# Optimization experiments

Measured on AMD Instinct MI355X. Metric: run time of the kernel, lower is better.

## Reference

```python
import jax, jax.numpy as jnp
import numpy as np

D_MODEL = 1024
NUM_HEADS = 16
HEAD_DIM = D_MODEL // NUM_HEADS
BATCH = 2
SEQ = 2048


def setup_inputs() -> dict:
    key = jax.random.key(0)
    ks = jax.random.split(key, 9)
    s_in = 1.0 / np.sqrt(D_MODEL)  # kaiming-ish fan-in scaling for stability
    return {
        "x": jax.random.normal(ks[0], (BATCH, SEQ, D_MODEL), jnp.float32),
        "wq": jax.random.normal(ks[1], (D_MODEL, D_MODEL), jnp.float32) * s_in,
        "bq": jnp.zeros((D_MODEL,), jnp.float32),
        "wk": jax.random.normal(ks[2], (D_MODEL, D_MODEL), jnp.float32) * s_in,
        "bk": jnp.zeros((D_MODEL,), jnp.float32),
        "wv": jax.random.normal(ks[3], (D_MODEL, D_MODEL), jnp.float32) * s_in,
        "bv": jnp.zeros((D_MODEL,), jnp.float32),
        "wo": jax.random.normal(ks[4], (D_MODEL, D_MODEL), jnp.float32) * s_in,
        "bo": jnp.zeros((D_MODEL,), jnp.float32),
    }


def reference(x, wq, bq, wk, bk, wv, bv, wo, bo):
    B, S, _ = x.shape
    # QKV projections, split heads: [B, H, S, Dh]
    def proj(w, b):
        y = x @ w + b
        return y.reshape(B, S, NUM_HEADS, HEAD_DIM).transpose(0, 2, 1, 3)

    q = proj(wq, bq)
    k = proj(wk, bk)
    v = proj(wv, bv)

    scale = 1.0 / jnp.sqrt(jnp.float32(HEAD_DIM))
    scores = jnp.einsum("bhsd,bhtd->bhst", q, k) * scale  # [B,H,S,S]
    attn = jax.nn.softmax(scores, axis=-1)
    out = jnp.einsum("bhst,bhtd->bhsd", attn, v)  # [B,H,S,Dh]
    out = out.transpose(0, 2, 1, 3).reshape(B, S, D_MODEL)
    return out @ wo + bo
```

## Files before the change

### kernel.cpp

```cpp
#include <hip/hip_runtime.h>
#include <stdint.h>
#include <stddef.h>


typedef __attribute__((ext_vector_type(8))) short short8;
typedef __attribute__((ext_vector_type(4))) float f32x4;
typedef __attribute__((ext_vector_type(16))) float f32x16;
typedef __attribute__((ext_vector_type(4))) unsigned short u16x4;
typedef _Float16 h4 __attribute__((ext_vector_type(4)));

#define MFMA16(a, b, c) __builtin_amdgcn_mfma_f32_16x16x32_bf16((a), (b), (c), 0, 0, 0)
#define MFMA32(a, b, c) __builtin_amdgcn_mfma_f32_32x32x16_bf16((a), (b), (c), 0, 0, 0)
#define AS1 __attribute__((address_space(1)))
#define AS3 __attribute__((address_space(3)))

__device__ __forceinline__ unsigned short f2bf(float f) {
  union { float f; unsigned u; } v; v.f = f;
  unsigned r = v.u + 0x7fffu + ((v.u >> 16) & 1u);
  return (unsigned short)(r >> 16);
}

__device__ __forceinline__ float fexp2(float x) {
#if __has_builtin(__builtin_amdgcn_exp2f)
  return __builtin_amdgcn_exp2f(x);
#else
  return __builtin_exp2f(x);
#endif
}

__device__ __forceinline__ unsigned cvt_pk_bf16(float lo, float hi) {
  unsigned r;
  asm("v_cvt_pk_bf16_f32 %0, %1, %2" : "=v"(r) : "v"(lo), "v"(hi));
  return r;
}

__device__ __forceinline__ void pl32_swap(unsigned& a, unsigned& b) {
  asm volatile("v_permlane32_swap_b32 %0, %1" : "+v"(a), "+v"(b));
}

__device__ __forceinline__ short8 mk8(unsigned a, unsigned b, unsigned c, unsigned d) {
  union { unsigned u[4]; short8 s; } v;
  v.u[0] = a; v.u[1] = b; v.u[2] = c; v.u[3] = d;
  return v.s;
}

__global__ __launch_bounds__(256) void prep_all_kernel(const float* __restrict__ x,
                                                       const float* __restrict__ wq,
                                                       const float* __restrict__ wk,
                                                       const float* __restrict__ wv,
                                                       const float* __restrict__ wo,
                                                       const float* __restrict__ bq,
                                                       const float* __restrict__ bk,
                                                       const float* __restrict__ bv,
                                                       unsigned short* __restrict__ xb,
                                                       unsigned short* __restrict__ wt,
                                                       float* __restrict__ bias3) {
  __shared__ unsigned short t_lds[32][33];
  const int bid = blockIdx.x;
  if (bid < 4096) {
    int wsel = bid >> 10;
    int rem = bid & 1023;
    int kb = (rem >> 5) << 5;
    int nb = (rem & 31) << 5;
    const float* W = (wsel == 0) ? wq : (wsel == 1) ? wk : (wsel == 2) ? wv : wo;
    int t = threadIdx.x;
    int r = t >> 3, c = (t & 7) * 4;
    float4 v = *reinterpret_cast<const float4*>(W + (size_t)(kb + r) * 1024 + nb + c);
    t_lds[r][c + 0] = f2bf(v.x);
    t_lds[r][c + 1] = f2bf(v.y);
    t_lds[r][c + 2] = f2bf(v.z);
    t_lds[r][c + 3] = f2bf(v.w);
    __syncthreads();
    u16x4 o;
    o.x = t_lds[c + 0][r]; o.y = t_lds[c + 1][r];
    o.z = t_lds[c + 2][r]; o.w = t_lds[c + 3][r];
    *reinterpret_cast<u16x4*>(wt + (size_t)(wsel * 1024 + nb + r) * 1024 + kb + c) = o;
  } else if (bid < 8192) {
    int i = ((bid - 4096) * 256 + threadIdx.x) * 4;
    float4 v = *reinterpret_cast<const float4*>(x + i);
    u16x4 o;
    o.x = f2bf(v.x); o.y = f2bf(v.y); o.z = f2bf(v.z); o.w = f2bf(v.w);
    *reinterpret_cast<u16x4*>(xb + i) = o;
  } else {
#pragma unroll
    for (int k = 0; k < 12; ++k) {
      int i = k * 256 + threadIdx.x;
      bias3[i] = (i < 1024) ? bq[i] : (i < 2048) ? bk[i - 1024] : bv[i - 2048];
    }
  }
}

template <typename OutT, bool QS>
__global__ __launch_bounds__(256) void gemm_bt_kernel(const unsigned short* __restrict__ A,
                                                      const unsigned short* __restrict__ Bt,
                                                      const float* __restrict__ bias,
                                                      OutT* __restrict__ C, int N) {
  constexpr int K = 1024;
  __shared__ __align__(16) unsigned short a_lds[2][128 * 32];
  __shared__ __align__(16) unsigned short b_lds[2][128 * 32];
  const int nb = N >> 7;
  const int nwg = nb << 5;
  const int cpx = nwg >> 3;
  const int wg = ((int)blockIdx.x & 7) * cpx + ((int)blockIdx.x >> 3);
  const int bm = wg / nb;
  const int bn = wg % nb;
  const int m0 = bm << 7, n0 = bn << 7;
  const int tid = threadIdx.x;
  const int w = tid >> 6, l = tid & 63;
  const int lr = l & 15, lg = l >> 4;
  const int wm = (w >> 1) << 6, wn = (w & 1) << 6;

  const int q0 = w * 2, q1 = w * 2 + 1;
  const unsigned short* pa0 = A + (size_t)(m0 + q0 * 16 + (l >> 2)) * K + (l & 3) * 8;
  const unsigned short* pa1 = A + (size_t)(m0 + q1 * 16 + (l >> 2)) * K + (l & 3) * 8;
  const unsigned short* pb0 = Bt + (size_t)(n0 + q0 * 16 + (l >> 2)) * K + (l & 3) * 8;
  const unsigned short* pb1 = Bt + (size_t)(n0 + q1 * 16 + (l >> 2)) * K + (l & 3) * 8;

#define GEMM_STAGE(buf, k0)                                                        \
  do {                                                                             \
    __builtin_amdgcn_global_load_lds((const AS1 void*)(pa0 + (k0)),                \
        (AS3 void*)(&a_lds[buf][q0 * 512]), 16, 0, 0);                             \
    __builtin_amdgcn_global_load_lds((const AS1 void*)(pa1 + (k0)),                \
        (AS3 void*)(&a_lds[buf][q1 * 512]), 16, 0, 0);                             \
    __builtin_amdgcn_global_load_lds((const AS1 void*)(pb0 + (k0)),                \
        (AS3 void*)(&b_lds[buf][q0 * 512]), 16, 0, 0);                             \
    __builtin_amdgcn_global_load_lds((const AS1 void*)(pb1 + (k0)),                \
        (AS3 void*)(&b_lds[buf][q1 * 512]), 16, 0, 0);                             \
  } while (0)

  f32x4 acc[4][4] = {};
  GEMM_STAGE(0, 0);
  __syncthreads();

  int cur = 0;
  for (int k0 = 0; k0 < K; k0 += 32) {
    if (k0 + 32 < K) GEMM_STAGE(cur ^ 1, k0 + 32);
    short8 af[4], bfr[4];
#pragma unroll
    for (int i = 0; i < 4; ++i)
      af[i] = *reinterpret_cast<const short8*>(&a_lds[cur][(wm + i * 16 + lr) * 32 + lg * 8]);
#pragma unroll
    for (int i = 0; i < 4; ++i)
      bfr[i] = *reinterpret_cast<const short8*>(&b_lds[cur][(wn + i * 16 + lr) * 32 + lg * 8]);
#pragma unroll
    for (int i = 0; i < 4; ++i)
#pragma unroll
      for (int j = 0; j < 4; ++j)
        acc[i][j] = MFMA16(af[i], bfr[j], acc[i][j]);
    __syncthreads();
    cur ^= 1;
  }
#undef GEMM_STAGE

  const float scale = (QS && n0 < 1024) ? 0.18033688011111f : 1.0f;
#pragma unroll
  for (int i = 0; i < 4; ++i) {
#pragma unroll
    for (int j = 0; j < 4; ++j) {
#pragma unroll
      for (int r = 0; r < 4; ++r) {
        int m = m0 + wm + i * 16 + lg * 4 + r;
        int n = n0 + wn + j * 16 + lr;
        float val = (acc[i][j][r] + bias[n]) * scale;
        if constexpr (sizeof(OutT) == 2) {
          C[(size_t)m * N + n] = (OutT)f2bf(val);
        } else {
          C[(size_t)m * N + n] = val;
        }
      }
    }
  }
}

__device__ __forceinline__ void stage_v(char* vw, int pi, int vd0, short8 va, short8 vb) {
  union { short8 s; unsigned u[4]; } ua, ub;
  ua.s = va; ub.s = vb;
#pragma unroll
  for (int jr = 0; jr < 4; ++jr) {
    unsigned w0 = __builtin_amdgcn_perm(ub.u[jr], ua.u[jr], 0x05040100u);
    unsigned w1 = __builtin_amdgcn_perm(ub.u[jr], ua.u[jr], 0x07060302u);
    int d0 = vd0 + 2 * jr, d1 = d0 + 1;
    *reinterpret_cast<unsigned*>(vw + d0 * 128 + ((4 * pi) ^ ((d0 & 7) << 4))) = w0;
    *reinterpret_cast<unsigned*>(vw + d1 * 128 + ((4 * pi) ^ ((d1 & 7) << 4))) = w1;
  }
}

template <int S>
__global__ __launch_bounds__(256, 4) void attn_kernel(const unsigned short* __restrict__ qkv,
                                                      _Float16* __restrict__ poA,
                                                      _Float16* __restrict__ poB,
                                                      float* __restrict__ pl) {
  constexpr int TLEN = 2048 / S;
  __shared__ __align__(16) unsigned short k_lds[2][64 * 64];
  __shared__ __align__(16) unsigned short vt_lds[2][64 * 64];
  const int tid = threadIdx.x;
  const int w = tid >> 6, l = tid & 63;
  const int lq = l & 31;
  const int hi = l >> 5;
  const int nwg = 512 * S;
  const int wg = ((int)blockIdx.x & 7) * (nwg >> 3) + ((int)blockIdx.x >> 3);
  int bh, qblk, kv;
  if (S == 2) { bh = wg >> 5; qblk = (wg >> 1) & 15; kv = wg & 1; }
  else        { bh = wg >> 4; qblk = wg & 15;        kv = 0; }
  const int b = bh >> 4, h = bh & 15;
  const size_t rowbase = (size_t)b * 2048;
  const int q0 = qblk * 128 + w * 32;

  short8 qf[4];
  {
    const unsigned short* qrow = qkv + (rowbase + q0 + lq) * 3072 + h * 64 + hi * 8;
#pragma unroll
    for (int c = 0; c < 4; ++c)
      qf[c] = *reinterpret_cast<const short8*>(qrow + c * 16);
  }

  const int colsw = (16 * (l & 7)) ^ ((l >> 3) << 4);
  const char* ksrc = (const char*)(qkv + (rowbase + kv * TLEN) * 3072 + 1024 + h * 64) +
                     (size_t)(16 * w + (l >> 3)) * 6144 + colsw;
  const int kdst = w * 2048;

  const int pi = tid & 31;
  const int vd0 = (tid >> 5) * 8;
  const unsigned short* vbase = qkv + (rowbase + kv * TLEN) * 3072 + 2048 + h * 64;
  const int swz_lq = (lq & 7) << 4;

  short8 ones;
  {
    union { unsigned u[4]; short8 s; } o_;
    o_.u[0] = o_.u[1] = o_.u[2] = o_.u[3] = 0x3F803F80u;
    ones = o_.s;
  }

  f32x16 ot0 = {}, ot1 = {}, lacc = {};

  __builtin_amdgcn_global_load_lds((const AS1 void*)ksrc,
                                   (AS3 void*)((char*)k_lds[0] + kdst), 16, 0, 0);
  __builtin_amdgcn_global_load_lds((const AS1 void*)(ksrc + 49152),
                                   (AS3 void*)((char*)k_lds[0] + kdst + 1024), 16, 0, 0);
  ksrc += 393216;
  {
    short8 va = *reinterpret_cast<const short8*>(vbase + (size_t)(2 * pi) * 3072 + vd0);
    short8 vb = *reinterpret_cast<const short8*>(vbase + (size_t)(2 * pi + 1) * 3072 + vd0);
    stage_v((char*)vt_lds[0], pi, vd0, va, vb);
  }

  int cur = 0;
  for (int t0 = 0; t0 < TLEN; t0 += 64) {
    __syncthreads();
    const bool more = (t0 + 64) < TLEN;
    short8 vna, vnb;
    if (more) {
      char* kd = (char*)k_lds[cur ^ 1] + kdst;
      __builtin_amdgcn_global_load_lds((const AS1 void*)ksrc, (AS3 void*)kd, 16, 0, 0);
      __builtin_amdgcn_global_load_lds((const AS1 void*)(ksrc + 49152),
                                       (AS3 void*)(kd + 1024), 16, 0, 0);
      ksrc += 393216;
      vna = *reinterpret_cast<const short8*>(vbase + (size_t)(t0 + 64 + 2 * pi) * 3072 + vd0);
      vnb = *reinterpret_cast<const short8*>(vbase + (size_t)(t0 + 65 + 2 * pi) * 3072 + vd0);
    }
    const char* kl = (const char*)k_lds[cur];
    const char* vl = (const char*)vt_lds[cur];

    f32x16 s0 = {}, s1 = {};
    __builtin_amdgcn_s_setprio(1);
#pragma unroll
    for (int c = 0; c < 4; ++c) {
      short8 kf0 = *reinterpret_cast<const short8*>(kl + lq * 128 + ((c * 32 + hi * 16) ^ swz_lq));
      short8 kf1 = *reinterpret_cast<const short8*>(kl + (32 + lq) * 128 + ((c * 32 + hi * 16) ^ swz_lq));
      s0 = MFMA32(kf0, qf[c], s0);
      s1 = MFMA32(kf1, qf[c], s1);
    }
    __builtin_amdgcn_s_setprio(0);

    if (more) stage_v((char*)vt_lds[cur ^ 1], pi, vd0, vna, vnb);

#pragma unroll
    for (int c = 0; c < 4; ++c) {
      float t0_, t1_, t2_, t3_, t4_, t5_, t6_, t7_;
      if (c < 2) {
        const int o = c * 8;
        t0_ = fexp2(s0[o + 0]); t1_ = fexp2(s0[o + 1]);
        t2_ = fexp2(s0[o + 2]); t3_ = fexp2(s0[o + 3]);
        t4_ = fexp2(s0[o + 4]); t5_ = fexp2(s0[o + 5]);
        t6_ = fexp2(s0[o + 6]); t7_ = fexp2(s0[o + 7]);
      } else {
        const int o = (c - 2) * 8;
        t0_ = fexp2(s1[o + 0]); t1_ = fexp2(s1[o + 1]);
        t2_ = fexp2(s1[o + 2]); t3_ = fexp2(s1[o + 3]);
        t4_ = fexp2(s1[o + 4]); t5_ = fexp2(s1[o + 5]);
        t6_ = fexp2(s1[o + 6]); t7_ = fexp2(s1[o + 7]);
      }
      unsigned a0 = cvt_pk_bf16(t0_, t1_), a1 = cvt_pk_bf16(t4_, t5_);
      unsigned b0 = cvt_pk_bf16(t2_, t3_), b1 = cvt_pk_bf16(t6_, t7_);
      pl32_swap(a0, a1); pl32_swap(b0, b1);
      short8 pfc = mk8(a0, b0, a1, b1);
      short8 vf0 = *reinterpret_cast<const short8*>(vl + lq * 128 + ((c * 32 + hi * 16) ^ swz_lq));
      short8 vf1 = *reinterpret_cast<const short8*>(vl + (32 + lq) * 128 + ((c * 32 + hi * 16) ^ swz_lq));
      __builtin_amdgcn_s_setprio(1);
      ot0 = MFMA32(vf0, pfc, ot0);
      ot1 = MFMA32(vf1, pfc, ot1);
      lacc = MFMA32(ones, pfc, lacc);
      __builtin_amdgcn_s_setprio(0);
    }
    cur ^= 1;
  }

  const int g = bh * 16 + qblk;
  _Float16* pop = (kv == 0 ? poA : poB) + (size_t)g * 8192;
#pragma unroll
  for (int r = 0; r < 16; ++r) {
    int d = (r & 3) + 8 * (r >> 2) + 4 * hi;
    pop[d * 128 + w * 32 + lq] = (_Float16)ot0[r];
    pop[(32 + d) * 128 + w * 32 + lq] = (_Float16)ot1[r];
  }
  if (hi == 0) pl[(size_t)(g * S + kv) * 128 + w * 32 + lq] = lacc[0];
}

template <int S>
__global__ __launch_bounds__(256) void merge_kernel(const _Float16* __restrict__ poA,
                                                    const _Float16* __restrict__ poB,
                                                    const float* __restrict__ pl,
                                                    unsigned short* __restrict__ aout) {
  __shared__ unsigned short lo[128][72];
  const int g = blockIdx.x;
  const int bh = g >> 4, qblk = g & 15;
  const int b = bh >> 4, h = bh & 15;
  const int tid = threadIdx.x;
  const int qi = (tid & 31) * 4;
  const int dg = tid >> 5;
  const _Float16* P0 = poA + (size_t)g * 8192;
  const _Float16* P1 = poB + (size_t)g * 8192;
  const float* L = pl + (size_t)g * S * 128;

  float inv[4];
#pragma unroll
  for (int j = 0; j < 4; ++j) {
    float lv = L[qi + j];
    if (S == 2) lv += L[128 + qi + j];
    inv[j] = 1.0f / lv;
  }
#pragma unroll
  for (int dd = 0; dd < 8; ++dd) {
    int d = dg * 8 + dd;
    h4 a = *reinterpret_cast<const h4*>(P0 + d * 128 + qi);
    float o[4];
#pragma unroll
    for (int j = 0; j < 4; ++j) o[j] = (float)a[j];
    if (S == 2) {
      h4 bb = *reinterpret_cast<const h4*>(P1 + d * 128 + qi);
#pragma unroll
      for (int j = 0; j < 4; ++j) o[j] += (float)bb[j];
    }
#pragma unroll
    for (int j = 0; j < 4; ++j) lo[qi + j][d] = f2bf(o[j] * inv[j]);
  }
  __syncthreads();
  const int q = tid >> 1, c0 = (tid & 1) * 32;
  unsigned short* orow = aout + (size_t)(b * 2048 + qblk * 128 + q) * 1024 + h * 64 + c0;
#pragma unroll
  for (int k = 0; k < 4; ++k)
    *reinterpret_cast<short8*>(orow + k * 8) =
        *reinterpret_cast<const short8*>(&lo[q][c0 + k * 8]);
}

extern "C" void kernel_launch(void* const* d_in, const int* in_sizes, int n_in,
                              void* d_out, int out_size, void* d_ws, size_t ws_size,
                              hipStream_t stream) {
  const float* x  = (const float*)d_in[0];
  const float* wq = (const float*)d_in[1];
  const float* bq = (const float*)d_in[2];
  const float* wk = (const float*)d_in[3];
  const float* bk = (const float*)d_in[4];
  const float* wv = (const float*)d_in[5];
  const float* bv = (const float*)d_in[6];
  const float* wo = (const float*)d_in[7];
  const float* bo = (const float*)d_in[8];
  float* out = (float*)d_out;

  char* ws = (char*)d_ws;
  unsigned short* xb    = (unsigned short*)(ws);
  _Float16*       poA   = (_Float16*)(ws);
  unsigned short* wt    = (unsigned short*)(ws + 8388608);
  float*          bias3 = (float*)(ws + 16777216);
  unsigned short* qkvb  = (unsigned short*)(ws + 16842752);
  unsigned short* aob   = qkvb;
  _Float16*       poB   = (_Float16*)(ws + 42008576);
  const bool s2 = ws_size >= (size_t)51500000;
  float* pl = (float*)(s2 ? (ws + 50397184) : (ws + 42008576));

  prep_all_kernel<<<8193, 256, 0, stream>>>(x, wq, wk, wv, wo, bq, bk, bv, xb, wt, bias3);

  gemm_bt_kernel<unsigned short, true><<<768, 256, 0, stream>>>(xb, wt, bias3, qkvb, 3072);

  if (s2) {
    attn_kernel<2><<<1024, 256, 0, stream>>>(qkvb, poA, poB, pl);
    merge_kernel<2><<<512, 256, 0, stream>>>(poA, poB, pl, aob);
  } else {
    attn_kernel<1><<<512, 256, 0, stream>>>(qkvb, poA, poB, pl);
    merge_kernel<1><<<512, 256, 0, stream>>>(poA, poB, pl, aob);
  }

  gemm_bt_kernel<float, false><<<256, 256, 0, stream>>>(aob, wt + (size_t)3072 * 1024, bo, out, 1024);
}
```

Baseline: 125.0 us.

## Split KV inside workgroup and merge partial attention outputs in LDS

Attention now runs as one 512-thread workgroup per query block. Two groups of four waves each process half of the key/value sequence. The partial outputs and row sums are combined through LDS at the end, and the normalized bf16 result is written straight to the attention output buffer. This removes the separate merge kernel, its launch, and the fp16 partial-output round trip through global memory. In exchange it uses 64KB of LDS per workgroup with larger blocks, which may limit occupancy, and adds extra barriers for the in-LDS reduction.

Measured after the change: 116.0 us. -7.2%, faster.

```diff
diff --git a/kernel.cpp b/kernel.cpp
--- a/kernel.cpp
+++ b/kernel.cpp
@@ -7,7 +7,6 @@
 typedef __attribute__((ext_vector_type(4))) float f32x4;
 typedef __attribute__((ext_vector_type(16))) float f32x16;
 typedef __attribute__((ext_vector_type(4))) unsigned short u16x4;
-typedef _Float16 h4 __attribute__((ext_vector_type(4)));
 
 #define MFMA16(a, b, c) __builtin_amdgcn_mfma_f32_16x16x32_bf16((a), (b), (c), 0, 0, 0)
 #define MFMA32(a, b, c) __builtin_amdgcn_mfma_f32_32x32x16_bf16((a), (b), (c), 0, 0, 0)
@@ -185,26 +184,20 @@
   }
 }
 
-template <int S>
-__global__ __launch_bounds__(256, 4) void attn_kernel(const unsigned short* __restrict__ qkv,
-                                                      _Float16* __restrict__ poA,
-                                                      _Float16* __restrict__ poB,
-                                                      float* __restrict__ pl) {
-  constexpr int TLEN = 2048 / S;
-  __shared__ __align__(16) unsigned short k_lds[2][64 * 64];
-  __shared__ __align__(16) unsigned short vt_lds[2][64 * 64];
+__global__ __launch_bounds__(512, 4) void attn_kernel(const unsigned short* __restrict__ qkv,
+                                                       unsigned short* __restrict__ aout) {
+  __shared__ __align__(16) char lds[65536];
   const int tid = threadIdx.x;
   const int w = tid >> 6, l = tid & 63;
+  const int kv = w >> 2, wsub = w & 3;
   const int lq = l & 31;
   const int hi = l >> 5;
-  const int nwg = 512 * S;
-  const int wg = ((int)blockIdx.x & 7) * (nwg >> 3) + ((int)blockIdx.x >> 3);
-  int bh, qblk, kv;
-  if (S == 2) { bh = wg >> 5; qblk = (wg >> 1) & 15; kv = wg & 1; }
-  else        { bh = wg >> 4; qblk = wg & 15;        kv = 0; }
+  const int wg = ((int)blockIdx.x & 7) * 64 + ((int)blockIdx.x >> 3);
+  const int bh = wg >> 4, qblk = wg & 15;
   const int b = bh >> 4, h = bh & 15;
   const size_t rowbase = (size_t)b * 2048;
-  const int q0 = qblk * 128 + w * 32;
+  const int q0 = qblk * 128 + wsub * 32;
+  const int base = kv << 15;
 
   short8 qf[4];
   {
@@ -215,13 +208,13 @@
   }
 
   const int colsw = (16 * (l & 7)) ^ ((l >> 3) << 4);
-  const char* ksrc = (const char*)(qkv + (rowbase + kv * TLEN) * 3072 + 1024 + h * 64) +
-                     (size_t)(16 * w + (l >> 3)) * 6144 + colsw;
-  const int kdst = w * 2048;
+  const char* ksrc = (const char*)(qkv + (rowbase + kv * 1024) * 3072 + 1024 + h * 64) +
+                     (size_t)(16 * wsub + (l >> 3)) * 6144 + colsw;
+  const int kdst = wsub * 2048;
 
   const int pi = tid & 31;
-  const int vd0 = (tid >> 5) * 8;
-  const unsigned short* vbase = qkv + (rowbase + kv * TLEN) * 3072 + 2048 + h * 64;
+  const int vd0 = ((tid >> 5) & 7) * 8;
+  const unsigned short* vbase = qkv + (rowbase + kv * 1024) * 3072 + 2048 + h * 64;
   const int swz_lq = (lq & 7) << 4;
 
   short8 ones;
@@ -234,23 +227,23 @@
   f32x16 ot0 = {}, ot1 = {}, lacc = {};
 
   __builtin_amdgcn_global_load_lds((const AS1 void*)ksrc,
-                                   (AS3 void*)((char*)k_lds[0] + kdst), 16, 0, 0);
+                                   (AS3 void*)(lds + base + kdst), 16, 0, 0);
   __builtin_amdgcn_global_load_lds((const AS1 void*)(ksrc + 49152),
-                                   (AS3 void*)((char*)k_lds[0] + kdst + 1024), 16, 0, 0);
+                                   (AS3 void*)(lds + base + kdst + 1024), 16, 0, 0);
   ksrc += 393216;
   {
     short8 va = *reinterpret_cast<const short8*>(vbase + (size_t)(2 * pi) * 3072 + vd0);
     short8 vb = *reinterpret_cast<const short8*>(vbase + (size_t)(2 * pi + 1) * 3072 + vd0);
-    stage_v((char*)vt_lds[0], pi, vd0, va, vb);
+    stage_v(lds + base + 16384, pi, vd0, va, vb);
   }
 
   int cur = 0;
-  for (int t0 = 0; t0 < TLEN; t0 += 64) {
+  for (int t0 = 0; t0 < 1024; t0 += 64) {
     __syncthreads();
-    const bool more = (t0 + 64) < TLEN;
+    const bool more = (t0 + 64) < 1024;
     short8 vna, vnb;
     if (more) {
-      char* kd = (char*)k_lds[cur ^ 1] + kdst;
+      char* kd = lds + base + ((cur ^ 1) << 13) + kdst;
       __builtin_amdgcn_global_load_lds((const AS1 void*)ksrc, (AS3 void*)kd, 16, 0, 0);
       __builtin_amdgcn_global_load_lds((const AS1 void*)(ksrc + 49152),
                                        (AS3 void*)(kd + 1024), 16, 0, 0);
@@ -258,8 +251,8 @@
       vna = *reinterpret_cast<const short8*>(vbase + (size_t)(t0 + 64 + 2 * pi) * 3072 + vd0);
       vnb = *reinterpret_cast<const short8*>(vbase + (size_t)(t0 + 65 + 2 * pi) * 3072 + vd0);
     }
-    const char* kl = (const char*)k_lds[cur];
-    const char* vl = (const char*)vt_lds[cur];
+    const char* kl = lds + base + (cur << 13);
+    const char* vl = lds + base + 16384 + (cur << 13);
 
     f32x16 s0 = {}, s1 = {};
     __builtin_amdgcn_s_setprio(1);
@@ -272,7 +265,7 @@
     }
     __builtin_amdgcn_s_setprio(0);
 
-    if (more) stage_v((char*)vt_lds[cur ^ 1], pi, vd0, vna, vnb);
+    if (more) stage_v(lds + base + 16384 + ((cur ^ 1) << 13), pi, vd0, vna, vnb);
 
 #pragma unroll
     for (int c = 0; c < 4; ++c) {
@@ -305,62 +298,48 @@
     cur ^= 1;
   }
 
-  const int g = bh * 16 + qblk;
-  _Float16* pop = (kv == 0 ? poA : poB) + (size_t)g * 8192;
-#pragma unroll
-  for (int r = 0; r < 16; ++r) {
-    int d = (r & 3) + 8 * (r >> 2) + 4 * hi;
-    pop[d * 128 + w * 32 + lq] = (_Float16)ot0[r];
-    pop[(32 + d) * 128 + w * 32 + lq] = (_Float16)ot1[r];
-  }
-  if (hi == 0) pl[(size_t)(g * S + kv) * 128 + w * 32 + lq] = lacc[0];
-}
-
-template <int S>
-__global__ __launch_bounds__(256) void merge_kernel(const _Float16* __restrict__ poA,
-                                                    const _Float16* __restrict__ poB,
-                                                    const float* __restrict__ pl,
-                                                    unsigned short* __restrict__ aout) {
-  __shared__ unsigned short lo[128][72];
-  const int g = blockIdx.x;
-  const int bh = g >> 4, qblk = g & 15;
-  const int b = bh >> 4, h = bh & 15;
-  const int tid = threadIdx.x;
-  const int qi = (tid & 31) * 4;
-  const int dg = tid >> 5;
-  const _Float16* P0 = poA + (size_t)g * 8192;
-  const _Float16* P1 = poB + (size_t)g * 8192;
-  const float* L = pl + (size_t)g * S * 128;
-
-  float inv[4];
-#pragma unroll
-  for (int j = 0; j < 4; ++j) {
-    float lv = L[qi + j];
-    if (S == 2) lv += L[128 + qi + j];
-    inv[j] = 1.0f / lv;
-  }
-#pragma unroll
-  for (int dd = 0; dd < 8; ++dd) {
-    int d = dg * 8 + dd;
-    h4 a = *reinterpret_cast<const h4*>(P0 + d * 128 + qi);
-    float o[4];
-#pragma unroll
-    for (int j = 0; j < 4; ++j) o[j] = (float)a[j];
-    if (S == 2) {
-      h4 bb = *reinterpret_cast<const h4*>(P1 + d * 128 + qi);
-#pragma unroll
-      for (int j = 0; j < 4; ++j) o[j] += (float)bb[j];
-    }
-#pragma unroll
-    for (int j = 0; j < 4; ++j) lo[qi + j][d] = f2bf(o[j] * inv[j]);
-  }
   __syncthreads();
-  const int q = tid >> 1, c0 = (tid & 1) * 32;
-  unsigned short* orow = aout + (size_t)(b * 2048 + qblk * 128 + q) * 1024 + h * 64 + c0;
-#pragma unroll
-  for (int k = 0; k < 4; ++k)
-    *reinterpret_cast<short8*>(orow + k * 8) =
-        *reinterpret_cast<const short8*>(&lo[q][c0 + k * 8]);
+  float* lbuf = (float*)lds;
+  if (kv == 1) {
+    float* ob = (float*)(lds + 32768 + wsub * 8192);
+#pragma unroll
+    for (int r = 0; r < 16; ++r) {
+      int d = (r & 3) + 8 * (r >> 2) + 4 * hi;
+      ob[d * 32 + lq] = ot0[r];
+      ob[(32 + d) * 32 + lq] = ot1[r];
+    }
+    if (hi == 0) lbuf[wsub * 32 + lq] = lacc[0];
+  }
+  __syncthreads();
+  if (kv == 0) {
+    const float* ob = (const float*)(lds + 32768 + wsub * 8192);
+    const float inv = 1.0f / (lacc[0] + lbuf[wsub * 32 + lq]);
+    char* st = lds + 8192;
+    const int qq = wsub * 32 + lq;
+    const int swz = (qq & 7) << 4;
+#pragma unroll
+    for (int r = 0; r < 16; r += 2) {
+      int d = (r & 3) + 8 * (r >> 2) + 4 * hi;
+      float a0 = (ot0[r] + ob[d * 32 + lq]) * inv;
+      float a1 = (ot0[r + 1] + ob[(d + 1) * 32 + lq]) * inv;
+      *(unsigned*)(st + qq * 128 + ((2 * d) ^ swz)) = cvt_pk_bf16(a0, a1);
+      float b0_ = (ot1[r] + ob[(32 + d) * 32 + lq]) * inv;
+      float b1_ = (ot1[r + 1] + ob[(33 + d) * 32 + lq]) * inv;
+      *(unsigned*)(st + qq * 128 + ((2 * (32 + d)) ^ swz)) = cvt_pk_bf16(b0_, b1_);
+    }
+  }
+  __syncthreads();
+  {
+    int row = tid >> 2;
+    int c2 = (tid & 3) * 2;
+    int swzr = (row & 7) << 4;
+    const char* src = lds + 8192 + row * 128;
+    short8 v0 = *reinterpret_cast<const short8*>(src + ((c2 * 16) ^ swzr));
+    short8 v1 = *reinterpret_cast<const short8*>(src + (((c2 + 1) * 16) ^ swzr));
+    unsigned short* orow = aout + (rowbase + qblk * 128 + row) * 1024 + h * 64 + c2 * 8;
+    *reinterpret_cast<short8*>(orow) = v0;
+    *reinterpret_cast<short8*>(orow + 8) = v1;
+  }
 }
 
 extern "C" void kernel_launch(void* const* d_in, const int* in_sizes, int n_in,
@@ -379,26 +358,16 @@
 
   char* ws = (char*)d_ws;
   unsigned short* xb    = (unsigned short*)(ws);
-  _Float16*       poA   = (_Float16*)(ws);
+  unsigned short* aob   = (unsigned short*)(ws);
   unsigned short* wt    = (unsigned short*)(ws + 8388608);
   float*          bias3 = (float*)(ws + 16777216);
   unsigned short* qkvb  = (unsigned short*)(ws + 16842752);
-  unsigned short* aob   = qkvb;
-  _Float16*       poB   = (_Float16*)(ws + 42008576);
-  const bool s2 = ws_size >= (size_t)51500000;
-  float* pl = (float*)(s2 ? (ws + 50397184) : (ws + 42008576));
 
   prep_all_kernel<<<8193, 256, 0, stream>>>(x, wq, wk, wv, wo, bq, bk, bv, xb, wt, bias3);
 
   gemm_bt_kernel<unsigned short, true><<<768, 256, 0, stream>>>(xb, wt, bias3, qkvb, 3072);
 
-  if (s2) {
-    attn_kernel<2><<<1024, 256, 0, stream>>>(qkvb, poA, poB, pl);
-    merge_kernel<2><<<512, 256, 0, stream>>>(poA, poB, pl, aob);
-  } else {
-    attn_kernel<1><<<512, 256, 0, stream>>>(qkvb, poA, poB, pl);
-    merge_kernel<1><<<512, 256, 0, stream>>>(poA, poB, pl, aob);
-  }
+  attn_kernel<<<512, 512, 0, stream>>>(qkvb, aob);
 
   gemm_bt_kernel<float, false><<<256, 256, 0, stream>>>(aob, wt + (size_t)3072 * 1024, bo, out, 1024);
 }
```
